# Optimization experiments

Measured on AMD Instinct MI355X. Metric: run time of the kernel, lower is better.

Reference implementation:

```python
import jax, jax.numpy as jnp
import numpy as np

D, FF, E, K = 1024, 1024, 8, 2  # d_model, ffn_dim, n_experts, top_k
B, S = 4, 1024


def _gelu(x):
    # torch F.gelu default is the exact erf form
    return jax.nn.gelu(x, approximate=False)


def setup_inputs() -> dict:
    key = jax.random.key(0)
    ks = jax.random.split(key, 12)
    s = 0.02
    return {
        "x": jax.random.normal(ks[0], (B, S, D), jnp.float32),
        "gate_w": jax.random.normal(ks[1], (D, E), jnp.float32) * s,
        "gate_b": jnp.zeros((E,), jnp.float32),
        # shared expert (n_shared = 1)
        "sw1": jax.random.normal(ks[2], (D, FF), jnp.float32) * s,
        "sb1": jnp.zeros((FF,), jnp.float32),
        "sw2": jax.random.normal(ks[3], (FF, D), jnp.float32) * s,
        "sb2": jnp.zeros((D,), jnp.float32),
        # routed experts, stacked over E
        "w1": jax.random.normal(ks[4], (E, D, FF), jnp.float32) * s,
        "b1": jnp.zeros((E, FF), jnp.float32),
        "w2": jax.random.normal(ks[5], (E, FF, D), jnp.float32) * s,
        "b2": jnp.zeros((E, D), jnp.float32),
    }


def reference(x, gate_w, gate_b, sw1, sb1, sw2, sb2, w1, b1, w2, b2):
    Bb, Ss, Dm = x.shape
    t = x.reshape(-1, Dm)  # [T, D]
    T = t.shape[0]

    # shared expert(s)
    shared = _gelu(t @ sw1 + sb1) @ sw2 + sb2  # [T, D]

    # gating: softmax over experts, then top-k
    probs = jax.nn.softmax(t @ gate_w + gate_b, axis=-1)  # [T, E]
    topk_p, topk_i = jax.lax.top_k(probs, K)  # [T, K]

    # combine weights: sparse [T, E] with top-k probs (top_k indices are distinct)
    combine = jnp.zeros((T, E), t.dtype).at[
        jnp.arange(T)[:, None], topk_i
    ].set(topk_p)

    # expert FFNs computed densely, combined with sparse routing weights;
    # mathematically identical to the masked gather-GEMM-scatter loop
    h = _gelu(jnp.einsum("td,edf->etf", t, w1) + b1[:, None, :])  # [E, T, FF]
    y = jnp.einsum("etf,efd->etd", h, w2) + b2[:, None, :]        # [E, T, D]
    routed = jnp.einsum("te,etd->td", combine, y)                  # [T, D]

    return (routed + shared).reshape(Bb, Ss, Dm)
```

## Files before the change

### kernel.cpp

```cpp
#include <hip/hip_runtime.h>
#include <hip/hip_bf16.h>


typedef short short8 __attribute__((ext_vector_type(8)));
typedef float f32x4  __attribute__((ext_vector_type(4)));

#define T_TOK 4096
#define NSLOT 8192
#define NWG   832
#define CHUNK 104

#define OFF_XB    (size_t)0
#define OFF_W1T   (size_t)8388608
#define OFF_W2T   (size_t)25165824
#define OFF_SW1T  (size_t)41943040
#define OFF_SW2T  (size_t)44040192
#define OFF_HS    (size_t)46137344
#define OFF_HR    (size_t)54525952
#define OFF_META  (size_t)73400320
#define OFF_ROWMAP (size_t)73400576
#define OFF_ROWW  (size_t)73437440
#define OFF_TKI   (size_t)73474304
#define OFF_TKP   (size_t)73507072

__device__ __forceinline__ unsigned short f2bf(float f) {
  __hip_bfloat16 h = __float2bfloat16(f);
  return __builtin_bit_cast(unsigned short, h);
}
__device__ __forceinline__ float gelu_exact(float x) {
  return 0.5f * x * (1.0f + erff(x * 0.70710678118654752f));
}

#define GLOAD16(g, l)                                                          \
  __builtin_amdgcn_global_load_lds(                                            \
      (const __attribute__((address_space(1))) void*)(g),                      \
      (__attribute__((address_space(3))) void*)(l), 16, 0, 0)


__global__ void k_transpose(const float* __restrict__ w1, const float* __restrict__ w2,
                            const float* __restrict__ sw1, const float* __restrict__ sw2,
                            unsigned short* __restrict__ w1t, unsigned short* __restrict__ w2t,
                            unsigned short* __restrict__ sw1t, unsigned short* __restrict__ sw2t) {
  __shared__ float tile[32][33];
  int z = blockIdx.z;
  const float* src; unsigned short* dst;
  if (z < 8)       { src = w1 + (size_t)z * 1048576;        dst = w1t + (size_t)z * 1048576; }
  else if (z < 16) { src = w2 + (size_t)(z - 8) * 1048576;  dst = w2t + (size_t)(z - 8) * 1048576; }
  else if (z == 16){ src = sw1; dst = sw1t; }
  else             { src = sw2; dst = sw2t; }
  int tx = threadIdx.x, ty = threadIdx.y;
  int gx = blockIdx.x * 32 + tx;
#pragma unroll
  for (int j = 0; j < 4; j++) {
    int gy = blockIdx.y * 32 + ty + j * 8;
    tile[ty + j * 8][tx] = src[(size_t)gy * 1024 + gx];
  }
  __syncthreads();
#pragma unroll
  for (int j = 0; j < 4; j++) {
    int orow = blockIdx.x * 32 + ty + j * 8;
    int ocol = blockIdx.y * 32 + tx;
    dst[(size_t)orow * 1024 + ocol] = f2bf(tile[tx][ty + j * 8]);
  }
}

__global__ void k_convert_x(const float* __restrict__ x, unsigned short* __restrict__ xb) {
  int i = blockIdx.x * blockDim.x + threadIdx.x;
  float4 v = ((const float4*)x)[i];
  ushort4 o;
  o.x = f2bf(v.x); o.y = f2bf(v.y); o.z = f2bf(v.z); o.w = f2bf(v.w);
  ((ushort4*)xb)[i] = o;
}

__global__ void k_gate(const float* __restrict__ x, const float* __restrict__ gw,
                       const float* __restrict__ gb, int* __restrict__ tki,
                       float* __restrict__ tkp) {
  int wv = threadIdx.x >> 6, l = threadIdx.x & 63;
  int t = blockIdx.x * 4 + wv;
  float acc[8] = {0, 0, 0, 0, 0, 0, 0, 0};
  const float* xr = x + (size_t)t * 1024;
#pragma unroll
  for (int j = 0; j < 16; j++) {
    int k = j * 64 + l;
    float xv = xr[k];
    const float4* g4 = (const float4*)(gw + (size_t)k * 8);
    float4 ga = g4[0], gbv = g4[1];
    acc[0] += xv * ga.x; acc[1] += xv * ga.y; acc[2] += xv * ga.z; acc[3] += xv * ga.w;
    acc[4] += xv * gbv.x; acc[5] += xv * gbv.y; acc[6] += xv * gbv.z; acc[7] += xv * gbv.w;
  }
#pragma unroll
  for (int off = 32; off > 0; off >>= 1) {
#pragma unroll
    for (int e = 0; e < 8; e++) acc[e] += __shfl_xor(acc[e], off);
  }
  if (l == 0) {
    float lg[8], p[8];
    float m = -1e30f;
#pragma unroll
    for (int e = 0; e < 8; e++) { lg[e] = acc[e] + gb[e]; m = fmaxf(m, lg[e]); }
    float s = 0.f;
#pragma unroll
    for (int e = 0; e < 8; e++) { p[e] = expf(lg[e] - m); s += p[e]; }
    float inv = 1.0f / s;
#pragma unroll
    for (int e = 0; e < 8; e++) p[e] *= inv;
    int i0 = 0;
#pragma unroll
    for (int e = 1; e < 8; e++) if (p[e] > p[i0]) i0 = e;
    int i1 = (i0 == 0) ? 1 : 0;
#pragma unroll
    for (int e = 0; e < 8; e++) if (e != i0 && p[e] > p[i1]) i1 = e;
    tki[t * 2] = i0; tki[t * 2 + 1] = i1;
    tkp[t * 2] = p[i0]; tkp[t * 2 + 1] = p[i1];
  }
}

__global__ void k_route(const int* __restrict__ tki, const float* __restrict__ tkp,
                        int* __restrict__ counts, int* __restrict__ basev,
                        int* __restrict__ rowmap, float* __restrict__ roww) {
  int e = blockIdx.x, tid = threadIdx.x;
  int lane = tid & 63, wv = tid >> 6;
  int c[8] = {0, 0, 0, 0, 0, 0, 0, 0};
  for (int i = tid; i < NSLOT; i += 256) {
    int v = tki[i];
#pragma unroll
    for (int q = 0; q < 8; q++) c[q] += (v == q);
  }
  __shared__ int red[8][64];
#pragma unroll
  for (int q = 0; q < 8; q++) {
#pragma unroll
    for (int off = 32; off > 0; off >>= 1) c[q] += __shfl_xor(c[q], off);
  }
  if (lane == 0) {
#pragma unroll
    for (int q = 0; q < 8; q++) red[q][wv] = c[q];
  }
  __syncthreads();
  __shared__ int cnt_s[8], base_s[8];
  if (tid == 0) {
    int off = 0;
#pragma unroll
    for (int q = 0; q < 8; q++) {
      int cq = red[q][0] + red[q][1] + red[q][2] + red[q][3];
      cnt_s[q] = cq; base_s[q] = off;
      off += (cq + 127) & ~127;
    }
    counts[e] = cnt_s[e];
    basev[e] = base_s[e];
  }
  __syncthreads();
  __shared__ int warpsum[4];
  int wpos = base_s[e];
  for (int i0 = 0; i0 < NSLOT; i0 += 256) {
    int i = i0 + tid;
    bool pred = (tki[i] == e);
    unsigned long long mask = __ballot(pred);
    int wpre = __popcll(mask & ((1ull << lane) - 1));
    if (lane == 0) warpsum[wv] = __popcll(mask);
    __syncthreads();
    int wbase = 0;
    for (int w = 0; w < wv; w++) wbase += warpsum[w];
    int total = warpsum[0] + warpsum[1] + warpsum[2] + warpsum[3];
    if (pred) {
      int pos = wpos + wbase + wpre;
      rowmap[pos] = i >> 1;
      roww[pos] = tkp[i];
    }
    wpos += total;
    __syncthreads();
  }
}

template <int PHASE>
__global__ __launch_bounds__(256, 4) void k_ffn(
    const unsigned short* __restrict__ As,
    const unsigned short* __restrict__ Ar,
    const unsigned short* __restrict__ Bsh, const float* __restrict__ bsh,
    const unsigned short* __restrict__ Brt, const float* __restrict__ brt,
    unsigned short* __restrict__ Hsh, unsigned short* __restrict__ Hrt,
    float* __restrict__ outf,
    const int* __restrict__ rowmap, const float* __restrict__ roww,
    const int* __restrict__ counts, const int* __restrict__ bases) {
  __shared__ unsigned short ldsA[128 * 64];
  __shared__ unsigned short ldsB[128 * 64];

  int bid = blockIdx.x;
  int j = (bid & 7) * CHUNK + (bid >> 3);
  int z = -1, rel = j;
  if (rel < 256) {
    z = 0;
  } else {
    rel -= 256;
#pragma unroll
    for (int e = 0; e < 8; e++) {
      int nye = ((counts[e] + 127) >> 7) << 3;
      if (z < 0) {
        if (rel < nye) z = e + 1; else rel -= nye;
      }
    }
    if (z < 0) return;
  }
  int row0 = (rel >> 3) * 128;
  int n0 = (rel & 7) * 128;

  int nrows, rbase = 0;
  const unsigned short* Bmat; const float* bvec; const unsigned short* Amat;
  if (z == 0) {
    nrows = T_TOK; Bmat = Bsh; bvec = bsh; Amat = As;
  } else {
    int e = z - 1;
    nrows = counts[e]; rbase = bases[e];
    Bmat = Brt + (size_t)e * 1048576;
    bvec = brt + (size_t)e * 1024;
    Amat = (PHASE == 1) ? As : Ar;
  }
  int tid = threadIdx.x, wave = tid >> 6, lane = tid & 63;
  int wm = wave >> 1, wn = wave & 1;

  long arow[4];
#pragma unroll
  for (int i = 0; i < 4; i++) {
    int q = i * 4 + wave;
    int m = (q * 64 + lane) >> 3;
    int r = row0 + m;
    if (r >= nrows) r = nrows - 1;
    if (z == 0)            arow[i] = r;
    else if (PHASE == 1)   arow[i] = rowmap[rbase + r];
    else                   arow[i] = rbase + r;
  }

  f32x4 acc[4][4];
#pragma unroll
  for (int i = 0; i < 4; i++)
#pragma unroll
    for (int j2 = 0; j2 < 4; j2++) acc[i][j2] = (f32x4){0.f, 0.f, 0.f, 0.f};

  for (int k0 = 0; k0 < 1024; k0 += 64) {
#pragma unroll
    for (int i = 0; i < 4; i++) {
      int q = i * 4 + wave;
      int c = q * 64 + lane;
      int m = c >> 3, s = c & 7;
      int ks = s ^ (m & 7);
      GLOAD16(Amat + arow[i] * 1024 + k0 + ks * 8, &ldsA[q * 512]);
    }
#pragma unroll
    for (int i = 0; i < 4; i++) {
      int q = i * 4 + wave;
      int c = q * 64 + lane;
      int n = c >> 3, s = c & 7;
      int ks = s ^ (n & 7);
      GLOAD16(Bmat + (size_t)(n0 + n) * 1024 + k0 + ks * 8, &ldsB[q * 512]);
    }
    __syncthreads();
#pragma unroll
    for (int kk = 0; kk < 2; kk++) {
      short8 af[4], bfr[4];
      int kc0 = kk * 4 + (lane >> 4);
#pragma unroll
      for (int fi = 0; fi < 4; fi++) {
        int m = wm * 64 + fi * 16 + (lane & 15);
        int slot = kc0 ^ (m & 7);
        af[fi] = *(const short8*)&ldsA[m * 64 + slot * 8];
      }
#pragma unroll
      for (int fj = 0; fj < 4; fj++) {
        int n = wn * 64 + fj * 16 + (lane & 15);
        int slot = kc0 ^ (n & 7);
        bfr[fj] = *(const short8*)&ldsB[n * 64 + slot * 8];
      }
#pragma unroll
      for (int fi = 0; fi < 4; fi++)
#pragma unroll
        for (int fj = 0; fj < 4; fj++)
          acc[fi][fj] = __builtin_amdgcn_mfma_f32_16x16x32_bf16(af[fi], bfr[fj], acc[fi][fj], 0, 0, 0);
    }
    __syncthreads();
  }

#pragma unroll
  for (int fi = 0; fi < 4; fi++) {
#pragma unroll
    for (int rg = 0; rg < 4; rg++) {
      int lr = wm * 64 + fi * 16 + (lane >> 4) * 4 + rg;
      int r = row0 + lr;
      if (r >= nrows) continue;
      if (PHASE == 1) {
        unsigned short* dst = (z == 0) ? (Hsh + (size_t)r * 1024)
                                       : (Hrt + (size_t)(rbase + r) * 1024);
#pragma unroll
        for (int fj = 0; fj < 4; fj++) {
          int col = n0 + wn * 64 + fj * 16 + (lane & 15);
          dst[col] = f2bf(gelu_exact(acc[fi][fj][rg] + bvec[col]));
        }
      } else {
        if (z == 0) {
#pragma unroll
          for (int fj = 0; fj < 4; fj++) {
            int col = n0 + wn * 64 + fj * 16 + (lane & 15);
            atomicAdd(&outf[(size_t)r * 1024 + col], acc[fi][fj][rg] + bvec[col]);
          }
        } else {
          int tok = rowmap[rbase + r];
          float p = roww[rbase + r];
#pragma unroll
          for (int fj = 0; fj < 4; fj++) {
            int col = n0 + wn * 64 + fj * 16 + (lane & 15);
            atomicAdd(&outf[(size_t)tok * 1024 + col], p * (acc[fi][fj][rg] + bvec[col]));
          }
        }
      }
    }
  }
}

extern "C" void kernel_launch(void* const* d_in, const int* in_sizes, int n_in,
                              void* d_out, int out_size, void* d_ws, size_t ws_size,
                              hipStream_t stream) {
  const float* x   = (const float*)d_in[0];
  const float* gw  = (const float*)d_in[1];
  const float* gb  = (const float*)d_in[2];
  const float* sw1 = (const float*)d_in[3];
  const float* sb1 = (const float*)d_in[4];
  const float* sw2 = (const float*)d_in[5];
  const float* sb2 = (const float*)d_in[6];
  const float* w1  = (const float*)d_in[7];
  const float* b1  = (const float*)d_in[8];
  const float* w2  = (const float*)d_in[9];
  const float* b2  = (const float*)d_in[10];
  float* out = (float*)d_out;
  char* ws = (char*)d_ws;

  unsigned short* xb   = (unsigned short*)(ws + OFF_XB);
  unsigned short* w1t  = (unsigned short*)(ws + OFF_W1T);
  unsigned short* w2t  = (unsigned short*)(ws + OFF_W2T);
  unsigned short* sw1t = (unsigned short*)(ws + OFF_SW1T);
  unsigned short* sw2t = (unsigned short*)(ws + OFF_SW2T);
  unsigned short* Hs   = (unsigned short*)(ws + OFF_HS);
  unsigned short* Hr   = (unsigned short*)(ws + OFF_HR);
  int*   counts = (int*)(ws + OFF_META);
  int*   basev  = counts + 8;
  int*   rowmap = (int*)(ws + OFF_ROWMAP);
  float* roww   = (float*)(ws + OFF_ROWW);
  int*   tki    = (int*)(ws + OFF_TKI);
  float* tkp    = (float*)(ws + OFF_TKP);

  hipMemsetAsync(out, 0, (size_t)out_size * sizeof(float), stream);
  k_transpose<<<dim3(32, 32, 18), dim3(32, 8), 0, stream>>>(w1, w2, sw1, sw2, w1t, w2t, sw1t, sw2t);
  k_convert_x<<<4096, 256, 0, stream>>>(x, xb);
  k_gate<<<1024, 256, 0, stream>>>(x, gw, gb, tki, tkp);
  k_route<<<8, 256, 0, stream>>>(tki, tkp, counts, basev, rowmap, roww);

  k_ffn<1><<<NWG, 256, 0, stream>>>(xb, xb, sw1t, sb1, w1t, b1, Hs, Hr,
                                    nullptr, rowmap, roww, counts, basev);
  k_ffn<2><<<NWG, 256, 0, stream>>>(Hs, Hr, sw2t, sb2, w2t, b2, nullptr, nullptr,
                                    out, rowmap, roww, counts, basev);
}
```

Before: 186.3 us.

## Split-K second FFN GEMM, fuse x conversion into gate, widen transpose

The second expert GEMM now splits K into two halves across twice as many workgroups, with only the first half adding the bias. Both halves accumulate into the output through the existing atomics. The bf16 conversion of x is folded into the gating kernel, removing a separate launch and a reread of x. The weight transpose uses 64x64 tiles with float4 loads and ushort4 stores. Split-K doubles the atomic traffic to the output in exchange for more parallelism on the mi355x.

```diff
diff --git a/kernel.cpp b/kernel.cpp
--- a/kernel.cpp
+++ b/kernel.cpp
@@ -7,8 +7,10 @@
 
 #define T_TOK 4096
 #define NSLOT 8192
-#define NWG   832
-#define CHUNK 104
+#define NWG1  832
+#define CHUNK1 104
+#define NWG2  1664
+#define CHUNK2 208
 
 #define OFF_XB    (size_t)0
 #define OFF_W1T   (size_t)8388608
@@ -41,48 +43,47 @@
                             const float* __restrict__ sw1, const float* __restrict__ sw2,
                             unsigned short* __restrict__ w1t, unsigned short* __restrict__ w2t,
                             unsigned short* __restrict__ sw1t, unsigned short* __restrict__ sw2t) {
-  __shared__ float tile[32][33];
+  __shared__ float tile[64][65];
   int z = blockIdx.z;
   const float* src; unsigned short* dst;
   if (z < 8)       { src = w1 + (size_t)z * 1048576;        dst = w1t + (size_t)z * 1048576; }
   else if (z < 16) { src = w2 + (size_t)(z - 8) * 1048576;  dst = w2t + (size_t)(z - 8) * 1048576; }
   else if (z == 16){ src = sw1; dst = sw1t; }
   else             { src = sw2; dst = sw2t; }
-  int tx = threadIdx.x, ty = threadIdx.y;
-  int gx = blockIdx.x * 32 + tx;
-#pragma unroll
-  for (int j = 0; j < 4; j++) {
-    int gy = blockIdx.y * 32 + ty + j * 8;
-    tile[ty + j * 8][tx] = src[(size_t)gy * 1024 + gx];
+  int t = threadIdx.x;
+  int r = t >> 2, c4 = t & 3;
+  int gx0 = blockIdx.x * 64, gy0 = blockIdx.y * 64;
+#pragma unroll
+  for (int it = 0; it < 4; it++) {
+    int col4 = it * 4 + c4;
+    float4 v = *(const float4*)&src[(size_t)(gy0 + r) * 1024 + gx0 + col4 * 4];
+    tile[r][col4 * 4 + 0] = v.x; tile[r][col4 * 4 + 1] = v.y;
+    tile[r][col4 * 4 + 2] = v.z; tile[r][col4 * 4 + 3] = v.w;
   }
   __syncthreads();
 #pragma unroll
-  for (int j = 0; j < 4; j++) {
-    int orow = blockIdx.x * 32 + ty + j * 8;
-    int ocol = blockIdx.y * 32 + tx;
-    dst[(size_t)orow * 1024 + ocol] = f2bf(tile[tx][ty + j * 8]);
-  }
-}
-
-__global__ void k_convert_x(const float* __restrict__ x, unsigned short* __restrict__ xb) {
-  int i = blockIdx.x * blockDim.x + threadIdx.x;
-  float4 v = ((const float4*)x)[i];
-  ushort4 o;
-  o.x = f2bf(v.x); o.y = f2bf(v.y); o.z = f2bf(v.z); o.w = f2bf(v.w);
-  ((ushort4*)xb)[i] = o;
+  for (int it = 0; it < 4; it++) {
+    int cc = (it * 4 + c4) * 4;
+    ushort4 o;
+    o.x = f2bf(tile[cc + 0][r]); o.y = f2bf(tile[cc + 1][r]);
+    o.z = f2bf(tile[cc + 2][r]); o.w = f2bf(tile[cc + 3][r]);
+    *(ushort4*)&dst[(size_t)(gx0 + r) * 1024 + gy0 + cc] = o;
+  }
 }
 
 __global__ void k_gate(const float* __restrict__ x, const float* __restrict__ gw,
                        const float* __restrict__ gb, int* __restrict__ tki,
-                       float* __restrict__ tkp) {
+                       float* __restrict__ tkp, unsigned short* __restrict__ xb) {
   int wv = threadIdx.x >> 6, l = threadIdx.x & 63;
   int t = blockIdx.x * 4 + wv;
   float acc[8] = {0, 0, 0, 0, 0, 0, 0, 0};
   const float* xr = x + (size_t)t * 1024;
+  unsigned short* xbr = xb + (size_t)t * 1024;
 #pragma unroll
   for (int j = 0; j < 16; j++) {
     int k = j * 64 + l;
     float xv = xr[k];
+    xbr[k] = f2bf(xv);
     const float4* g4 = (const float4*)(gw + (size_t)k * 8);
     float4 ga = g4[0], gbv = g4[1];
     acc[0] += xv * ga.x; acc[1] += xv * ga.y; acc[2] += xv * ga.z; acc[3] += xv * ga.w;
@@ -172,7 +173,7 @@
   }
 }
 
-template <int PHASE>
+template <int PHASE, int KSPLIT>
 __global__ __launch_bounds__(256, 4) void k_ffn(
     const unsigned short* __restrict__ As,
     const unsigned short* __restrict__ Ar,
@@ -186,8 +187,11 @@
   __shared__ unsigned short ldsB[128 * 64];
 
   int bid = blockIdx.x;
-  int j = (bid & 7) * CHUNK + (bid >> 3);
-  int z = -1, rel = j;
+  int chunk = (KSPLIT == 2) ? CHUNK2 : CHUNK1;
+  int j = (bid & 7) * chunk + (bid >> 3);
+  int ks = (KSPLIT == 2) ? (j & 1) : 0;
+  int rel = (KSPLIT == 2) ? (j >> 1) : j;
+  int z = -1;
   if (rel < 256) {
     z = 0;
   } else {
@@ -217,6 +221,7 @@
   }
   int tid = threadIdx.x, wave = tid >> 6, lane = tid & 63;
   int wm = wave >> 1, wn = wave & 1;
+  int l15 = lane & 15, lh = lane >> 4;
 
   long arow[4];
 #pragma unroll
@@ -236,37 +241,39 @@
 #pragma unroll
     for (int j2 = 0; j2 < 4; j2++) acc[i][j2] = (f32x4){0.f, 0.f, 0.f, 0.f};
 
-  for (int k0 = 0; k0 < 1024; k0 += 64) {
+  int kbase = (KSPLIT == 2) ? ks * 512 : 0;
+  int kend = kbase + 1024 / KSPLIT;
+  for (int k0 = kbase; k0 < kend; k0 += 64) {
 #pragma unroll
     for (int i = 0; i < 4; i++) {
       int q = i * 4 + wave;
       int c = q * 64 + lane;
       int m = c >> 3, s = c & 7;
-      int ks = s ^ (m & 7);
-      GLOAD16(Amat + arow[i] * 1024 + k0 + ks * 8, &ldsA[q * 512]);
+      int ksw = s ^ (m & 7);
+      GLOAD16(Amat + arow[i] * 1024 + k0 + ksw * 8, &ldsA[q * 512]);
     }
 #pragma unroll
     for (int i = 0; i < 4; i++) {
       int q = i * 4 + wave;
       int c = q * 64 + lane;
       int n = c >> 3, s = c & 7;
-      int ks = s ^ (n & 7);
-      GLOAD16(Bmat + (size_t)(n0 + n) * 1024 + k0 + ks * 8, &ldsB[q * 512]);
+      int ksw = s ^ (n & 7);
+      GLOAD16(Bmat + (size_t)(n0 + n) * 1024 + k0 + ksw * 8, &ldsB[q * 512]);
     }
     __syncthreads();
 #pragma unroll
     for (int kk = 0; kk < 2; kk++) {
       short8 af[4], bfr[4];
-      int kc0 = kk * 4 + (lane >> 4);
+      int kc0 = kk * 4 + lh;
 #pragma unroll
       for (int fi = 0; fi < 4; fi++) {
-        int m = wm * 64 + fi * 16 + (lane & 15);
+        int m = wm * 64 + fi * 16 + l15;
         int slot = kc0 ^ (m & 7);
         af[fi] = *(const short8*)&ldsA[m * 64 + slot * 8];
       }
 #pragma unroll
       for (int fj = 0; fj < 4; fj++) {
-        int n = wn * 64 + fj * 16 + (lane & 15);
+        int n = wn * 64 + fj * 16 + l15;
         int slot = kc0 ^ (n & 7);
         bfr[fj] = *(const short8*)&ldsB[n * 64 + slot * 8];
       }
@@ -283,7 +290,7 @@
   for (int fi = 0; fi < 4; fi++) {
 #pragma unroll
     for (int rg = 0; rg < 4; rg++) {
-      int lr = wm * 64 + fi * 16 + (lane >> 4) * 4 + rg;
+      int lr = wm * 64 + fi * 16 + lh * 4 + rg;
       int r = row0 + lr;
       if (r >= nrows) continue;
       if (PHASE == 1) {
@@ -291,23 +298,25 @@
                                        : (Hrt + (size_t)(rbase + r) * 1024);
 #pragma unroll
         for (int fj = 0; fj < 4; fj++) {
-          int col = n0 + wn * 64 + fj * 16 + (lane & 15);
+          int col = n0 + wn * 64 + fj * 16 + l15;
           dst[col] = f2bf(gelu_exact(acc[fi][fj][rg] + bvec[col]));
         }
       } else {
         if (z == 0) {
 #pragma unroll
           for (int fj = 0; fj < 4; fj++) {
-            int col = n0 + wn * 64 + fj * 16 + (lane & 15);
-            atomicAdd(&outf[(size_t)r * 1024 + col], acc[fi][fj][rg] + bvec[col]);
+            int col = n0 + wn * 64 + fj * 16 + l15;
+            float v = acc[fi][fj][rg] + ((ks == 0) ? bvec[col] : 0.f);
+            atomicAdd(&outf[(size_t)r * 1024 + col], v);
           }
         } else {
           int tok = rowmap[rbase + r];
           float p = roww[rbase + r];
 #pragma unroll
           for (int fj = 0; fj < 4; fj++) {
-            int col = n0 + wn * 64 + fj * 16 + (lane & 15);
-            atomicAdd(&outf[(size_t)tok * 1024 + col], p * (acc[fi][fj][rg] + bvec[col]));
+            int col = n0 + wn * 64 + fj * 16 + l15;
+            float v = p * (acc[fi][fj][rg] + ((ks == 0) ? bvec[col] : 0.f));
+            atomicAdd(&outf[(size_t)tok * 1024 + col], v);
           }
         }
       }
@@ -347,13 +356,12 @@
   float* tkp    = (float*)(ws + OFF_TKP);
 
   hipMemsetAsync(out, 0, (size_t)out_size * sizeof(float), stream);
-  k_transpose<<<dim3(32, 32, 18), dim3(32, 8), 0, stream>>>(w1, w2, sw1, sw2, w1t, w2t, sw1t, sw2t);
-  k_convert_x<<<4096, 256, 0, stream>>>(x, xb);
-  k_gate<<<1024, 256, 0, stream>>>(x, gw, gb, tki, tkp);
+  k_transpose<<<dim3(16, 16, 18), 256, 0, stream>>>(w1, w2, sw1, sw2, w1t, w2t, sw1t, sw2t);
+  k_gate<<<1024, 256, 0, stream>>>(x, gw, gb, tki, tkp, xb);
   k_route<<<8, 256, 0, stream>>>(tki, tkp, counts, basev, rowmap, roww);
 
-  k_ffn<1><<<NWG, 256, 0, stream>>>(xb, xb, sw1t, sb1, w1t, b1, Hs, Hr,
-                                    nullptr, rowmap, roww, counts, basev);
-  k_ffn<2><<<NWG, 256, 0, stream>>>(Hs, Hr, sw2t, sb2, w2t, b2, nullptr, nullptr,
-                                    out, rowmap, roww, counts, basev);
-}
+  k_ffn<1, 1><<<NWG1, 256, 0, stream>>>(xb, xb, sw1t, sb1, w1t, b1, Hs, Hr,
+                                        nullptr, rowmap, roww, counts, basev);
+  k_ffn<2, 2><<<NWG2, 256, 0, stream>>>(Hs, Hr, sw2t, sb2, w2t, b2, nullptr, nullptr,
+                                        out, rowmap, roww, counts, basev);
+}
```

New measurement: 223.6 us. +20.0%, slower.
